# Performance work log

Hardware: AMD Instinct MI355X
Metric: run time of the kernel (lower is better)

## Reference

```python
import jax, jax.numpy as jnp
import numpy as np

N = 4            # polynomial points per segment
SEGMENTS = 32
LENGTH = 2.0
HALF = 0.5 * LENGTH
IN_CH = 32
OUT_CH = 32
BATCH = 16
NODES = 1024


def _cheb_points(n):
    # Chebyshev-Lobatto points on [-1, 1] (LagrangePoly basis nodes)
    return -np.cos(np.pi * np.arange(n) / (n - 1))


def setup_inputs() -> dict:
    key = jax.random.key(0)
    k1, k2 = jax.random.split(key)
    x = jax.random.normal(k1, (BATCH, IN_CH, NODES), dtype=jnp.float32)
    # w.data.uniform_(-weight_magnitude, weight_magnitude)
    w = jax.random.uniform(k2, (OUT_CH, IN_CH, (N - 1) * SEGMENTS + 1),
                           dtype=jnp.float32, minval=-1.0, maxval=1.0)
    return {"x": x, "w": w}


def _lagrange_basis(x_in):
    # x_in: [b, c, m] -> basis values [b, c, m, n]
    X = jnp.asarray(_cheb_points(N), dtype=x_in.dtype)
    cols = []
    for j in range(N):
        b = jnp.ones_like(x_in)
        for m in range(N):
            if m != j:
                b = b * (x_in - X[m]) / (X[j] - X[m])
        cols.append(b)
    return jnp.stack(cols, axis=-1)


def reference(x, w):
    # bin index per element, clamped to valid segments
    id_min = jnp.clip(((x + HALF) / LENGTH * SEGMENTS).astype(jnp.int32), 0, SEGMENTS - 1)
    id_max = id_min + 1
    wid_min = id_min * (N - 1)                         # [b, c, m]
    idx = wid_min[..., None] + jnp.arange(N)           # [b, c, m, n]
    c_idx = jnp.arange(IN_CH)[None, :, None, None]     # broadcast channel index
    wg = w[:, c_idx, idx]                              # [o, b, c, m, n] irregular gather
    wg = jnp.transpose(wg, (1, 0, 2, 3, 4))            # [b, o, c, m, n]
    # map x into the local segment coordinate in [-half, half]
    x_min = id_min.astype(x.dtype) / SEGMENTS * 2.0 - 1.0
    x_max = id_max.astype(x.dtype) / SEGMENTS * 2.0 - 1.0
    x_in = LENGTH * (x - x_min) / (x_max - x_min) - HALF
    basis = _lagrange_basis(x_in)                      # [b, c, m, n]
    # sum over in_channels and polynomial points -> [b, o, m]
    return jnp.einsum('bcmj,bocmj->bom', basis, wg)
```

## Files before the change

### kernel.cpp

```cpp
#include <hip/hip_runtime.h>

#define NB 16
#define NC 32
#define NO 32
#define NM 1024
#define SEGS 32
#define WLEN 97
#define MTB 64

#define WLDS_BYTES   131072
#define BLDS_BYTES   16384
#define SLDS_BYTES   4096
#define SMEM_BYTES   (WLDS_BYTES + BLDS_BYTES + SLDS_BYTES)

__device__ __forceinline__ unsigned f2bf(float f) {
    unsigned u = __float_as_uint(f);
    return (u + 0x7fffu + ((u >> 16) & 1u)) >> 16;
}

__global__ __launch_bounds__(256) void repack_w_kernel(const float* __restrict__ w,
                                                       uint2* __restrict__ w4) {
    int i = blockIdx.x * blockDim.x + threadIdx.x;
    if (i >= NC * SEGS * NO) return;
    int o   = i & 31;
    int seg = (i >> 5) & 31;
    int c   = i >> 10;
    const float* p = w + (o * NC + c) * WLEN + 3 * seg;
    unsigned b0 = f2bf(p[0]);
    unsigned b1 = f2bf(p[1]);
    unsigned b2 = f2bf(p[2]);
    unsigned b3 = f2bf(p[3]);
    w4[i] = make_uint2(b0 | (b1 << 16), b2 | (b3 << 16));
}

__device__ __forceinline__ float4 lagrange_basis(float xv, int& id_out) {
    float v  = (xv + 1.0f) * 16.0f;
    int   id = (int)v;
    id = min(max(id, 0), SEGS - 1);
    const float x_min = (float)id * 0.0625f - 1.0f;
    const float t     = (xv - x_min) * 32.0f - 1.0f;
    const float d0 = t + 1.0f;
    const float d1 = t + 0.5f;
    const float d2 = t - 0.5f;
    const float d3 = t - 1.0f;
    float4 bb;
    bb.x = d1 * d2 * d3 * (-0.66666667f);
    bb.y = d0 * d2 * d3 * ( 1.33333333f);
    bb.z = d0 * d1 * d3 * (-1.33333333f);
    bb.w = d0 * d1 * d2 * ( 0.66666667f);
    id_out = id;
    return bb;
}

__global__ __launch_bounds__(1024, 4) void pw_main_kernel(const float* __restrict__ x,
                                                          const uint2* __restrict__ w4,
                                                          float* __restrict__ out) {
    extern __shared__ char smem[];
    uint2*  wlds = (uint2*)smem;
    float4* blds = (float4*)(smem + WLDS_BYTES);
    int*    slds = (int*)(smem + WLDS_BYTES + BLDS_BYTES);
    float*  alds = (float*)(smem + WLDS_BYTES);

    const int blk = blockIdx.x;
    const int b   = blk >> 4;
    const int m0  = (blk & 15) * MTB;

    const int t     = threadIdx.x;
    const int o     = t & 31;
    const int mslot = t >> 5;

    float acc0 = 0.0f, acc1 = 0.0f;

#pragma unroll
    for (int p = 0; p < 2; ++p) {
        if (p) __syncthreads();

        {
            const uint4* src = (const uint4*)(w4 + (size_t)p * 16 * SEGS * NO);
            uint4* dst = (uint4*)wlds;
#pragma unroll
            for (int k = 0; k < 8; ++k) dst[t + 1024 * k] = src[t + 1024 * k];
        }

        {
            const int cp = t >> 6;
            const int m  = t & 63;
            const float xv = x[(b * NC + p * 16 + cp) * NM + m0 + m];
            int id;
            float4 bb = lagrange_basis(xv, id);
            blds[cp * 64 + m] = bb;
            slds[m * 16 + cp] = ((cp * SEGS + id) * NO) * 8;
        }
        __syncthreads();

        int4 offA[4], offB[4];
        {
            const int4* s0 = (const int4*)&slds[mslot * 16];
            const int4* s1 = (const int4*)&slds[(mslot + 32) * 16];
#pragma unroll
            for (int k = 0; k < 4; ++k) { offA[k] = s0[k]; offB[k] = s1[k]; }
        }

        const char* wb = (const char*)wlds;
#pragma unroll
        for (int k = 0; k < 4; ++k) {
            const int4 oa = offA[k];
            const int4 ob = offB[k];
#pragma unroll
            for (int j = 0; j < 4; ++j) {
                const int cp = 4 * k + j;
                const int ba = (j == 0) ? oa.x : (j == 1) ? oa.y : (j == 2) ? oa.z : oa.w;
                const int bbo = (j == 0) ? ob.x : (j == 1) ? ob.y : (j == 2) ? ob.z : ob.w;
                const float4 B0 = blds[cp * 64 + mslot];
                const float4 B1 = blds[cp * 64 + mslot + 32];
                const uint2 pa = *(const uint2*)(wb + ba + o * 8);
                const uint2 pb = *(const uint2*)(wb + bbo + o * 8);
                acc0 = fmaf(B0.x, __uint_as_float(pa.x << 16), acc0);
                acc0 = fmaf(B0.y, __uint_as_float(pa.x & 0xffff0000u), acc0);
                acc0 = fmaf(B0.z, __uint_as_float(pa.y << 16), acc0);
                acc0 = fmaf(B0.w, __uint_as_float(pa.y & 0xffff0000u), acc0);
                acc1 = fmaf(B1.x, __uint_as_float(pb.x << 16), acc1);
                acc1 = fmaf(B1.y, __uint_as_float(pb.x & 0xffff0000u), acc1);
                acc1 = fmaf(B1.z, __uint_as_float(pb.y << 16), acc1);
                acc1 = fmaf(B1.w, __uint_as_float(pb.y & 0xffff0000u), acc1);
            }
        }
    }

    __syncthreads();
    alds[o * 66 + mslot]      = acc0;
    alds[o * 66 + mslot + 32] = acc1;
    __syncthreads();
    {
        const int o2 = t >> 5;
        const int mw = t & 31;
        float2 r;
        r.x = alds[o2 * 66 + 2 * mw];
        r.y = alds[o2 * 66 + 2 * mw + 1];
        *(float2*)&out[(b * NO + o2) * NM + m0 + 2 * mw] = r;
    }
}

__global__ __launch_bounds__(256) void pw_fallback_kernel(const float* __restrict__ x,
                                                          const float* __restrict__ w,
                                                          float* __restrict__ out) {
    const int blk = blockIdx.x;
    const int b   = blk >> 7;
    const int m   = (blk & 127) * 8 + (threadIdx.x & 7);
    const int o   = threadIdx.x >> 3;

    float acc = 0.0f;
    for (int c = 0; c < NC; ++c) {
        const float xv = x[(b * NC + c) * NM + m];
        int id;
        float4 bb = lagrange_basis(xv, id);
        const float* p = w + (o * NC + c) * WLEN + 3 * id;
        acc = fmaf(bb.x, p[0], acc);
        acc = fmaf(bb.y, p[1], acc);
        acc = fmaf(bb.z, p[2], acc);
        acc = fmaf(bb.w, p[3], acc);
    }
    out[(b * NO + o) * NM + m] = acc;
}

extern "C" void kernel_launch(void* const* d_in, const int* in_sizes, int n_in,
                              void* d_out, int out_size, void* d_ws, size_t ws_size,
                              hipStream_t stream) {
    const float* x = (const float*)d_in[0];
    const float* w = (const float*)d_in[1];
    float* out = (float*)d_out;

    const size_t w4_bytes = (size_t)NC * SEGS * NO * sizeof(uint2);

    static bool attr_set = false;
    (void)attr_set;
    hipError_t err = hipFuncSetAttribute((const void*)pw_main_kernel,
                                         hipFuncAttributeMaxDynamicSharedMemorySize,
                                         SMEM_BYTES);

    if (err == hipSuccess && ws_size >= w4_bytes) {
        uint2* w4 = (uint2*)d_ws;
        repack_w_kernel<<<(NC * SEGS * NO + 255) / 256, 256, 0, stream>>>(w, w4);
        pw_main_kernel<<<NB * (NM / MTB), 1024, SMEM_BYTES, stream>>>(x, w4, out);
    } else {
        pw_fallback_kernel<<<NB * (NM / 8), 256, 0, stream>>>(x, w, out);
    }
}
```

Measured before the change: 64.66 us.

## Double-buffer weight staging with async global-to-LDS loads over eight channel phases

Replaces the two-pass staging of 128KB of packed weights into LDS with an eight-phase double-buffered pipeline. Each phase moves 32KB using global_load_lds, while the previous buffer is being consumed. All basis values and offsets are now computed once up front. The thread mapping changes so each thread produces two adjacent output channels with a single 16-byte LDS read. The LDS footprint shrinks, but the kernel adds a barrier per phase and relies on async LDS loads completing before each barrier.

Result: no change. 65.12 us (+0.7%).

```diff
diff --git a/kernel.cpp b/kernel.cpp
--- a/kernel.cpp
+++ b/kernel.cpp
@@ -7,15 +7,23 @@
 #define SEGS 32
 #define WLEN 97
 #define MTB 64
+#define NPH 8
+#define CPH 4
 
-#define WLDS_BYTES   131072
-#define BLDS_BYTES   16384
-#define SLDS_BYTES   4096
-#define SMEM_BYTES   (WLDS_BYTES + BLDS_BYTES + SLDS_BYTES)
+#define WBUF_BYTES 32768
+#define BLDS_OFF   65536
+#define SOFF_OFF   98304
+#define SMEM_BYTES 107520
 
 __device__ __forceinline__ unsigned f2bf(float f) {
     unsigned u = __float_as_uint(f);
     return (u + 0x7fffu + ((u >> 16) & 1u)) >> 16;
+}
+
+__device__ __forceinline__ void gld_lds16(const void* g, void* l) {
+    __builtin_amdgcn_global_load_lds(
+        (const __attribute__((address_space(1))) void*)g,
+        (__attribute__((address_space(3))) void*)l, 16, 0, 0);
 }
 
 __global__ __launch_bounds__(256) void repack_w_kernel(const float* __restrict__ w,
@@ -56,88 +64,88 @@
                                                           const uint2* __restrict__ w4,
                                                           float* __restrict__ out) {
     extern __shared__ char smem[];
-    uint2*  wlds = (uint2*)smem;
-    float4* blds = (float4*)(smem + WLDS_BYTES);
-    int*    slds = (int*)(smem + WLDS_BYTES + BLDS_BYTES);
-    float*  alds = (float*)(smem + WLDS_BYTES);
+    char* const wbuf0 = smem;
+    char* const wbuf1 = smem + WBUF_BYTES;
+    float4*     blds  = (float4*)(smem + BLDS_OFF);
+    int*        soff  = (int*)(smem + SOFF_OFF);
+    float*      alds  = (float*)smem;
 
     const int blk = blockIdx.x;
     const int b   = blk >> 4;
     const int m0  = (blk & 15) * MTB;
 
-    const int t     = threadIdx.x;
-    const int o     = t & 31;
-    const int mslot = t >> 5;
+    const int t    = threadIdx.x;
+    const int lane = t & 63;
+    const int wv   = t >> 6;
+    const int o2   = t & 15;
+    const int ms   = t >> 4;
+
+    const char* gw = (const char*)w4;
+
+    {
+        char* ld = wbuf0 + wv * 2048;
+        const char* gs = gw + wv * 2048 + lane * 16;
+        gld_lds16(gs, ld);
+        gld_lds16(gs + 1024, ld + 1024);
+    }
+
+#pragma unroll
+    for (int k = 0; k < 2; ++k) {
+        const int task = t + 1024 * k;
+        const int c = task >> 6;
+        const int m = task & 63;
+        const float xv = x[(b * NC + c) * NM + m0 + m];
+        int id;
+        float4 bb = lagrange_basis(xv, id);
+        blds[c * 64 + m] = bb;
+        soff[m * 36 + c] = (c & 3) * 8192 + id * 256;
+    }
+    __syncthreads();
 
     float acc0 = 0.0f, acc1 = 0.0f;
 
 #pragma unroll
-    for (int p = 0; p < 2; ++p) {
-        if (p) __syncthreads();
+    for (int ph = 0; ph < NPH; ++ph) {
+        const char* wb = (ph & 1) ? wbuf1 : wbuf0;
 
-        {
-            const uint4* src = (const uint4*)(w4 + (size_t)p * 16 * SEGS * NO);
-            uint4* dst = (uint4*)wlds;
-#pragma unroll
-            for (int k = 0; k < 8; ++k) dst[t + 1024 * k] = src[t + 1024 * k];
+        if (ph < NPH - 1) {
+            char* ld = ((ph & 1) ? wbuf0 : wbuf1) + wv * 2048;
+            const char* gs = gw + (ph + 1) * WBUF_BYTES + wv * 2048 + lane * 16;
+            gld_lds16(gs, ld);
+            gld_lds16(gs + 1024, ld + 1024);
         }
 
-        {
-            const int cp = t >> 6;
-            const int m  = t & 63;
-            const float xv = x[(b * NC + p * 16 + cp) * NM + m0 + m];
-            int id;
-            float4 bb = lagrange_basis(xv, id);
-            blds[cp * 64 + m] = bb;
-            slds[m * 16 + cp] = ((cp * SEGS + id) * NO) * 8;
+        const int4 off4 = *(const int4*)&soff[ms * 36 + ph * CPH];
+
+#pragma unroll
+        for (int j = 0; j < 4; ++j) {
+            const int offb = (j == 0) ? off4.x : (j == 1) ? off4.y
+                           : (j == 2) ? off4.z : off4.w;
+            const int c = ph * CPH + j;
+            const float4 bb = blds[c * 64 + ms];
+            const uint4  pw = *(const uint4*)(wb + offb + o2 * 16);
+            acc0 = fmaf(bb.x, __uint_as_float(pw.x << 16), acc0);
+            acc0 = fmaf(bb.y, __uint_as_float(pw.x & 0xffff0000u), acc0);
+            acc0 = fmaf(bb.z, __uint_as_float(pw.y << 16), acc0);
+            acc0 = fmaf(bb.w, __uint_as_float(pw.y & 0xffff0000u), acc0);
+            acc1 = fmaf(bb.x, __uint_as_float(pw.z << 16), acc1);
+            acc1 = fmaf(bb.y, __uint_as_float(pw.z & 0xffff0000u), acc1);
+            acc1 = fmaf(bb.z, __uint_as_float(pw.w << 16), acc1);
+            acc1 = fmaf(bb.w, __uint_as_float(pw.w & 0xffff0000u), acc1);
         }
         __syncthreads();
-
-        int4 offA[4], offB[4];
-        {
-            const int4* s0 = (const int4*)&slds[mslot * 16];
-            const int4* s1 = (const int4*)&slds[(mslot + 32) * 16];
-#pragma unroll
-            for (int k = 0; k < 4; ++k) { offA[k] = s0[k]; offB[k] = s1[k]; }
-        }
-
-        const char* wb = (const char*)wlds;
-#pragma unroll
-        for (int k = 0; k < 4; ++k) {
-            const int4 oa = offA[k];
-            const int4 ob = offB[k];
-#pragma unroll
-            for (int j = 0; j < 4; ++j) {
-                const int cp = 4 * k + j;
-                const int ba = (j == 0) ? oa.x : (j == 1) ? oa.y : (j == 2) ? oa.z : oa.w;
-                const int bbo = (j == 0) ? ob.x : (j == 1) ? ob.y : (j == 2) ? ob.z : ob.w;
-                const float4 B0 = blds[cp * 64 + mslot];
-                const float4 B1 = blds[cp * 64 + mslot + 32];
-                const uint2 pa = *(const uint2*)(wb + ba + o * 8);
-                const uint2 pb = *(const uint2*)(wb + bbo + o * 8);
-                acc0 = fmaf(B0.x, __uint_as_float(pa.x << 16), acc0);
-                acc0 = fmaf(B0.y, __uint_as_float(pa.x & 0xffff0000u), acc0);
-                acc0 = fmaf(B0.z, __uint_as_float(pa.y << 16), acc0);
-                acc0 = fmaf(B0.w, __uint_as_float(pa.y & 0xffff0000u), acc0);
-                acc1 = fmaf(B1.x, __uint_as_float(pb.x << 16), acc1);
-                acc1 = fmaf(B1.y, __uint_as_float(pb.x & 0xffff0000u), acc1);
-                acc1 = fmaf(B1.z, __uint_as_float(pb.y << 16), acc1);
-                acc1 = fmaf(B1.w, __uint_as_float(pb.y & 0xffff0000u), acc1);
-            }
-        }
     }
 
-    __syncthreads();
-    alds[o * 66 + mslot]      = acc0;
-    alds[o * 66 + mslot + 32] = acc1;
+    alds[(2 * o2) * 66 + ms]     = acc0;
+    alds[(2 * o2 + 1) * 66 + ms] = acc1;
     __syncthreads();
     {
-        const int o2 = t >> 5;
+        const int oo = t >> 5;
         const int mw = t & 31;
         float2 r;
-        r.x = alds[o2 * 66 + 2 * mw];
-        r.y = alds[o2 * 66 + 2 * mw + 1];
-        *(float2*)&out[(b * NO + o2) * NM + m0 + 2 * mw] = r;
+        r.x = alds[oo * 66 + 2 * mw];
+        r.y = alds[oo * 66 + 2 * mw + 1];
+        *(float2*)&out[(b * NO + oo) * NM + m0 + 2 * mw] = r;
     }
 }
 
@@ -172,8 +180,6 @@
 
     const size_t w4_bytes = (size_t)NC * SEGS * NO * sizeof(uint2);
 
-    static bool attr_set = false;
-    (void)attr_set;
     hipError_t err = hipFuncSetAttribute((const void*)pw_main_kernel,
                                          hipFuncAttributeMaxDynamicSharedMemorySize,
                                          SMEM_BYTES);
```
